# Optimization experiments

Measured on AMD Instinct MI355X. Metric: run time of the kernel, lower is better.

The kernel has to match this reference:

```python
import jax, jax.numpy as jnp
import numpy as np


def _pool2(x):
    # 2x2 max pool, stride 2 (matches F.max_pool2d(x, 2))
    b, c, h, w = x.shape
    return x.reshape(b, c, h // 2, 2, w // 2, 2).max(axis=(3, 5))


def setup_inputs() -> dict:
    key = jax.random.key(0)
    ks = jax.random.split(key, 6)
    B, C, H, W = 16, 512, 64, 64
    x = jax.random.normal(ks[0], (B, C, H, W), dtype=jnp.float32)
    scale = 0.02
    theta_w = jax.random.normal(ks[1], (C // 8, C), dtype=jnp.float32) * scale
    phi_w = jax.random.normal(ks[2], (C // 8, C), dtype=jnp.float32) * scale
    g_w = jax.random.normal(ks[3], (C // 2, C), dtype=jnp.float32) * scale
    o_w = jax.random.normal(ks[4], (C, C // 2), dtype=jnp.float32) * scale
    # original inits gamma=0; use a nonzero value so output depends on attention path
    gamma = jax.random.normal(ks[5], (), dtype=jnp.float32) * 0.5
    return {"x": x, "theta_w": theta_w, "phi_w": phi_w, "g_w": g_w, "o_w": o_w, "gamma": gamma}


def reference(x, theta_w, phi_w, g_w, o_w, gamma):
    B, C, H, W = x.shape
    HW = H * W
    # 1x1 convs == channel GEMMs
    theta = jnp.einsum('bchw,kc->bkhw', x, theta_w).reshape(B, C // 8, HW).transpose(0, 2, 1)  # [B, HW, C/8]
    phi = _pool2(jnp.einsum('bchw,kc->bkhw', x, phi_w)).reshape(B, C // 8, HW // 4)            # [B, C/8, HW/4]
    beta = jax.nn.softmax(jnp.einsum('bnk,bkm->bnm', theta, phi), axis=-1)                     # [B, HW, HW/4]
    g = _pool2(jnp.einsum('bchw,kc->bkhw', x, g_w)).reshape(B, C // 2, HW // 4)                # [B, C/2, HW/4]
    # g.bmm(beta^T): contract over pooled positions m -> [B, C/2, HW]
    o_in = jnp.einsum('bcm,bnm->bcn', g, beta).reshape(B, C // 2, H, W)
    o = jnp.einsum('bchw,kc->bkhw', o_in, o_w)                                                 # [B, C, H, W]
    return gamma * o + x
```

## Files before the change

kernel.cpp:

```cpp
#include <hip/hip_runtime.h>

#define B_   16
#define C_   512
#define HW_  4096
#define M_   1024
#define TPAD 136

typedef __attribute__((ext_vector_type(8))) short bf16x8;
typedef __attribute__((ext_vector_type(4))) float f32x4;

static __device__ __forceinline__ unsigned short f2bf(float f) {
    union { float f; unsigned u; } v; v.f = f;
    unsigned r = v.u + 0x7fffu + ((v.u >> 16) & 1u);
    return (unsigned short)(r >> 16);
}
static __device__ __forceinline__ float bf2f(unsigned short h) {
    union { unsigned u; float f; } v; v.u = ((unsigned)h) << 16;
    return v.f;
}
static __device__ __forceinline__ void gload_lds16(const void* g, void* l) {
    __builtin_amdgcn_global_load_lds(
        (const __attribute__((address_space(1))) unsigned int*)g,
        (__attribute__((address_space(3))) unsigned int*)l, 16, 0, 0);
}

__global__ __launch_bounds__(256) void k_weights(
    const float* __restrict__ thw, const float* __restrict__ phw,
    const float* __restrict__ gw,  const float* __restrict__ ow,
    unsigned short* __restrict__ Wb, unsigned short* __restrict__ oWb) {
    int i = blockIdx.x * 256 + threadIdx.x;
    if (i < 32768)        Wb[i] = f2bf(thw[i]);
    else if (i < 65536)   Wb[i] = f2bf(phw[i - 32768]);
    else if (i < 196608)  Wb[i] = f2bf(gw[i - 65536]);
    else if (i < 327680)  oWb[i - 196608] = f2bf(ow[i - 196608]);
}

__global__ __launch_bounds__(256) void k_transpose_x(
    const float* __restrict__ x, unsigned short* __restrict__ xT) {
    __shared__ float tile[64][65];
    int b = blockIdx.z, c0 = blockIdx.y * 64, hw0 = blockIdx.x * 64;
    const float* xb = x + ((size_t)b * C_ + c0) * HW_ + hw0;
    int t = threadIdx.x;
    int r = t >> 4, c4 = (t & 15) * 4;
#pragma unroll
    for (int k = 0; k < 4; k++) {
        int row = r + k * 16;
        float4 v = *reinterpret_cast<const float4*>(xb + (size_t)row * HW_ + c4);
        tile[row][c4 + 0] = v.x; tile[row][c4 + 1] = v.y;
        tile[row][c4 + 2] = v.z; tile[row][c4 + 3] = v.w;
    }
    __syncthreads();
    unsigned short* o = xT + ((size_t)b * HW_ + hw0) * C_ + c0;
#pragma unroll
    for (int k = 0; k < 4; k++) {
        int hwr = r + k * 16;
        ushort4 u;
        u.x = f2bf(tile[c4 + 0][hwr]); u.y = f2bf(tile[c4 + 1][hwr]);
        u.z = f2bf(tile[c4 + 2][hwr]); u.w = f2bf(tile[c4 + 3][hwr]);
        *reinterpret_cast<ushort4*>(o + (size_t)hwr * C_ + c4) = u;
    }
}

__global__ __launch_bounds__(256, 4) void k_proj(
    const unsigned short* __restrict__ xT, const unsigned short* __restrict__ Wb,
    unsigned short* __restrict__ theta_n, unsigned short* __restrict__ phi_p,
    unsigned short* __restrict__ g_p) {
    __shared__ unsigned short smem[128 * TPAD];
    unsigned short* As = smem;
    unsigned short* Bs = smem + 8192;

    int b = blockIdx.z, mt = blockIdx.y, bx = blockIdx.x;
    int hw0 = bx * 128;
    int tid = threadIdx.x, w = tid >> 6, lane = tid & 63;
    int l15 = lane & 15, q = lane >> 4;
    int wr = w >> 1, wc = w & 1;

    const unsigned short* Ab = Wb + (size_t)(mt * 128) * 512;
    const unsigned short* Bb = xT + ((size_t)b * HW_ + hw0) * 512;
    int trow = tid >> 3, tch = tid & 7;

    f32x4 acc[4][4] = {};
    for (int ks = 0; ks < 8; ks++) {
        int k0 = ks * 64;
        if (ks) __syncthreads();
#pragma unroll
        for (int i = 0; i < 4; i++) {
            int row = i * 32 + trow;
            int ch = tch ^ (row & 7);
            gload_lds16(Ab + (size_t)row * 512 + k0 + ch * 8, &As[(i * 256 + w * 64) * 8]);
        }
#pragma unroll
        for (int i = 0; i < 4; i++) {
            int row = i * 32 + trow;
            int ch = tch ^ (row & 7);
            gload_lds16(Bb + (size_t)row * 512 + k0 + ch * 8, &Bs[(i * 256 + w * 64) * 8]);
        }
        __syncthreads();
#pragma unroll
        for (int kk = 0; kk < 2; kk++) {
            bf16x8 af[4], bfr[4];
#pragma unroll
            for (int mi = 0; mi < 4; mi++) {
                int row = wr * 64 + mi * 16 + l15;
                int ch = (kk * 4 + q) ^ (row & 7);
                af[mi] = *(const bf16x8*)&As[row * 64 + ch * 8];
            }
#pragma unroll
            for (int ni = 0; ni < 4; ni++) {
                int row = wc * 64 + ni * 16 + l15;
                int ch = (kk * 4 + q) ^ (row & 7);
                bfr[ni] = *(const bf16x8*)&Bs[row * 64 + ch * 8];
            }
#pragma unroll
            for (int mi = 0; mi < 4; mi++)
#pragma unroll
                for (int ni = 0; ni < 4; ni++)
                    acc[mi][ni] = __builtin_amdgcn_mfma_f32_16x16x32_bf16(
                        af[mi], bfr[ni], acc[mi][ni], 0, 0, 0);
        }
    }

    __syncthreads();
#pragma unroll
    for (int mi = 0; mi < 4; mi++)
#pragma unroll
        for (int ni = 0; ni < 4; ni++) {
            int col = wc * 64 + ni * 16 + l15;
            int row = wr * 64 + mi * 16 + q * 4;
            ushort4 u;
            u.x = f2bf(acc[mi][ni][0]); u.y = f2bf(acc[mi][ni][1]);
            u.z = f2bf(acc[mi][ni][2]); u.w = f2bf(acc[mi][ni][3]);
            *reinterpret_cast<ushort4*>(&smem[col * TPAD + row]) = u;
        }
    __syncthreads();

    if (mt == 0) {
        int hw_l = tid >> 1, kh = (tid & 1) * 32;
        const unsigned short* srcp = &smem[hw_l * TPAD + kh];
        unsigned short* dstp = theta_n + ((size_t)b * HW_ + hw0 + hw_l) * 64 + kh;
#pragma unroll
        for (int i = 0; i < 4; i++)
            *reinterpret_cast<uint4*>(dstp + i * 8) =
                *reinterpret_cast<const uint4*>(srcp + i * 8);
        int pc = tid & 63, mg = tid >> 6;
#pragma unroll
        for (int j = 0; j < 8; j++) {
            int m_l = mg * 8 + j, w_ = m_l * 2;
            float v0 = bf2f(smem[(w_)      * TPAD + 64 + pc]);
            float v1 = bf2f(smem[(w_ + 1)  * TPAD + 64 + pc]);
            float v2 = bf2f(smem[(64 + w_) * TPAD + 64 + pc]);
            float v3 = bf2f(smem[(65 + w_) * TPAD + 64 + pc]);
            float v = fmaxf(fmaxf(v0, v1), fmaxf(v2, v3));
            phi_p[((size_t)b * M_ + bx * 32 + m_l) * 64 + pc] = f2bf(v);
        }
    } else {
        int lr = tid & 127, half = tid >> 7;
        int gc = (mt - 1) * 128 + lr;
        unsigned short* dst = g_p + ((size_t)b * 256 + gc) * M_ + bx * 32 + half * 16;
        unsigned short tmp[16];
#pragma unroll
        for (int i = 0; i < 16; i++) {
            int w_ = (half * 16 + i) * 2;
            float v0 = bf2f(smem[(w_)      * TPAD + lr]);
            float v1 = bf2f(smem[(w_ + 1)  * TPAD + lr]);
            float v2 = bf2f(smem[(64 + w_) * TPAD + lr]);
            float v3 = bf2f(smem[(65 + w_) * TPAD + lr]);
            tmp[i] = f2bf(fmaxf(fmaxf(v0, v1), fmaxf(v2, v3)));
        }
#pragma unroll
        for (int i = 0; i < 4; i++)
            *reinterpret_cast<ushort4*>(dst + i * 4) =
                *reinterpret_cast<const ushort4*>(&tmp[i * 4]);
    }
}

__global__ __launch_bounds__(256, 2) void k_attn(
    const unsigned short* __restrict__ theta_n, const unsigned short* __restrict__ phi_p,
    const unsigned short* __restrict__ g_p, unsigned short* __restrict__ o_in) {
    __shared__ unsigned short phi_s[64 * 64];
    __shared__ unsigned short g_s[256 * 64];
    __shared__ unsigned short p_lds[4][32][68];

    int b = blockIdx.y, n0 = blockIdx.x * 128;
    int tid = threadIdx.x, w = tid >> 6, lane = tid & 63;
    int l15 = lane & 15, q = lane >> 4;
    int nw = n0 + w * 32;

    const unsigned short* th = theta_n + ((size_t)b * HW_ + nw + l15) * 64 + q * 8;
    bf16x8 a[2][2];
    a[0][0] = *(const bf16x8*)(th);            a[0][1] = *(const bf16x8*)(th + 32);
    a[1][0] = *(const bf16x8*)(th + 16 * 64);  a[1][1] = *(const bf16x8*)(th + 16 * 64 + 32);

    const unsigned short* phib = phi_p + (size_t)b * M_ * 64;
    const unsigned short* gb   = g_p   + (size_t)b * 256 * M_;

    bf16x8 ones;
    {
        short v = (l15 == 0) ? (short)0x3F80 : (short)0;
#pragma unroll
        for (int i = 0; i < 8; i++) ones[i] = v;
    }

    int sw = l15 & 7;

    f32x4 acc[2][17] = {};
    for (int mc = 0; mc < 16; mc++) {
        int m0 = mc * 64;
        __syncthreads();
#pragma unroll
        for (int i = 0; i < 2; i++) {
            int u = i * 256 + tid;
            int row = u >> 3, ch = (lane & 7) ^ (row & 7);
            gload_lds16(phib + (size_t)(m0 + row) * 64 + ch * 8,
                        &phi_s[(i * 256 + w * 64) * 8]);
        }
#pragma unroll
        for (int i = 0; i < 8; i++) {
            int u = i * 256 + tid;
            int row = u >> 3, ch = (lane & 7) ^ (row & 7);
            gload_lds16(gb + (size_t)row * M_ + m0 + ch * 8,
                        &g_s[(i * 256 + w * 64) * 8]);
        }
        __syncthreads();

#pragma unroll
        for (int f = 0; f < 4; f++) {
            const unsigned short* pr = &phi_s[(f * 16 + l15) * 64];
            bf16x8 b0 = *(const bf16x8*)(pr + (q ^ sw) * 8);
            bf16x8 b1 = *(const bf16x8*)(pr + ((q + 4) ^ sw) * 8);
#pragma unroll
            for (int t = 0; t < 2; t++) {
                f32x4 s = {};
                s = __builtin_amdgcn_mfma_f32_16x16x32_bf16(a[t][0], b0, s, 0, 0, 0);
                s = __builtin_amdgcn_mfma_f32_16x16x32_bf16(a[t][1], b1, s, 0, 0, 0);
#pragma unroll
                for (int j = 0; j < 4; j++)
                    p_lds[w][t * 16 + q * 4 + j][f * 16 + l15] = f2bf(__expf(s[j]));
            }
        }
        bf16x8 p[2][2];
#pragma unroll
        for (int t = 0; t < 2; t++) {
            p[t][0] = *(const bf16x8*)&p_lds[w][t * 16 + l15][q * 8];
            p[t][1] = *(const bf16x8*)&p_lds[w][t * 16 + l15][32 + q * 8];
        }
#pragma unroll
        for (int cf = 0; cf < 16; cf++) {
            const unsigned short* gr = &g_s[(cf * 16 + l15) * 64];
            bf16x8 g0 = *(const bf16x8*)(gr + (q ^ sw) * 8);
            bf16x8 g1 = *(const bf16x8*)(gr + ((q + 4) ^ sw) * 8);
#pragma unroll
            for (int t = 0; t < 2; t++) {
                acc[t][cf] = __builtin_amdgcn_mfma_f32_16x16x32_bf16(p[t][0], g0, acc[t][cf], 0, 0, 0);
                acc[t][cf] = __builtin_amdgcn_mfma_f32_16x16x32_bf16(p[t][1], g1, acc[t][cf], 0, 0, 0);
            }
        }
#pragma unroll
        for (int t = 0; t < 2; t++) {
            acc[t][16] = __builtin_amdgcn_mfma_f32_16x16x32_bf16(p[t][0], ones, acc[t][16], 0, 0, 0);
            acc[t][16] = __builtin_amdgcn_mfma_f32_16x16x32_bf16(p[t][1], ones, acc[t][16], 0, 0, 0);
        }
    }

#pragma unroll
    for (int t = 0; t < 2; t++) {
        float dinv[4];
#pragma unroll
        for (int j = 0; j < 4; j++) {
            float d = __shfl(acc[t][16][j], (lane & 48), 64);
            dinv[j] = 1.0f / d;
        }
#pragma unroll
        for (int cf = 0; cf < 16; cf++)
#pragma unroll
            for (int j = 0; j < 4; j++)
                o_in[((size_t)b * HW_ + nw + t * 16 + q * 4 + j) * 256 + cf * 16 + l15] =
                    f2bf(acc[t][cf][j] * dinv[j]);
    }
}

__global__ __launch_bounds__(256, 4) void k_oproj(
    const unsigned short* __restrict__ o_in, const unsigned short* __restrict__ oWb,
    const float* __restrict__ x, const float* __restrict__ gamma_p,
    float* __restrict__ out) {
    __shared__ unsigned short smem[128 * TPAD];
    unsigned short* As = smem;
    unsigned short* Bs = smem + 8192;

    int b = blockIdx.z, mt = blockIdx.y, hw0 = blockIdx.x * 128;
    int tid = threadIdx.x, w = tid >> 6, lane = tid & 63;
    int l15 = lane & 15, q = lane >> 4;
    int wr = w >> 1, wc = w & 1;

    const unsigned short* Ab = oWb + (size_t)(mt * 128) * 256;
    const unsigned short* Bb = o_in + ((size_t)b * HW_ + hw0) * 256;
    int trow = tid >> 3, tch = tid & 7;

    f32x4 acc[4][4] = {};
    for (int ks = 0; ks < 4; ks++) {
        int k0 = ks * 64;
        if (ks) __syncthreads();
#pragma unroll
        for (int i = 0; i < 4; i++) {
            int row = i * 32 + trow;
            int ch = tch ^ (row & 7);
            gload_lds16(Ab + (size_t)row * 256 + k0 + ch * 8, &As[(i * 256 + w * 64) * 8]);
        }
#pragma unroll
        for (int i = 0; i < 4; i++) {
            int row = i * 32 + trow;
            int ch = tch ^ (row & 7);
            gload_lds16(Bb + (size_t)row * 256 + k0 + ch * 8, &Bs[(i * 256 + w * 64) * 8]);
        }
        __syncthreads();
#pragma unroll
        for (int kk = 0; kk < 2; kk++) {
            bf16x8 af[4], bfr[4];
#pragma unroll
            for (int mi = 0; mi < 4; mi++) {
                int row = wr * 64 + mi * 16 + l15;
                int ch = (kk * 4 + q) ^ (row & 7);
                af[mi] = *(const bf16x8*)&As[row * 64 + ch * 8];
            }
#pragma unroll
            for (int ni = 0; ni < 4; ni++) {
                int row = wc * 64 + ni * 16 + l15;
                int ch = (kk * 4 + q) ^ (row & 7);
                bfr[ni] = *(const bf16x8*)&Bs[row * 64 + ch * 8];
            }
#pragma unroll
            for (int mi = 0; mi < 4; mi++)
#pragma unroll
                for (int ni = 0; ni < 4; ni++)
                    acc[mi][ni] = __builtin_amdgcn_mfma_f32_16x16x32_bf16(
                        af[mi], bfr[ni], acc[mi][ni], 0, 0, 0);
        }
    }

    __syncthreads();
#pragma unroll
    for (int mi = 0; mi < 4; mi++)
#pragma unroll
        for (int ni = 0; ni < 4; ni++) {
            int col = wc * 64 + ni * 16 + l15;
            int rb = wr * 64 + mi * 16 + q * 4;
#pragma unroll
            for (int j = 0; j < 4; j++)
                smem[(rb + j) * TPAD + col] = f2bf(acc[mi][ni][j]);
        }
    __syncthreads();

    float gam = *gamma_p;
    int sub = tid >> 5, p32 = tid & 31;
#pragma unroll
    for (int p = 0; p < 16; p++) {
        int row = p * 8 + sub;
        ushort4 v = *reinterpret_cast<const ushort4*>(&smem[row * TPAD + p32 * 4]);
        size_t idx = ((size_t)b * C_ + mt * 128 + row) * HW_ + hw0 + p32 * 4;
        float4 xv = *reinterpret_cast<const float4*>(x + idx);
        float4 o;
        o.x = gam * bf2f(v.x) + xv.x;
        o.y = gam * bf2f(v.y) + xv.y;
        o.z = gam * bf2f(v.z) + xv.z;
        o.w = gam * bf2f(v.w) + xv.w;
        *reinterpret_cast<float4*>(out + idx) = o;
    }
}

extern "C" void kernel_launch(void* const* d_in, const int* in_sizes, int n_in,
                              void* d_out, int out_size, void* d_ws, size_t ws_size,
                              hipStream_t stream) {
    const float* x     = (const float*)d_in[0];
    const float* thw   = (const float*)d_in[1];
    const float* phw   = (const float*)d_in[2];
    const float* gw    = (const float*)d_in[3];
    const float* ow    = (const float*)d_in[4];
    const float* gamma = (const float*)d_in[5];
    float* out = (float*)d_out;

    char* ws = (char*)d_ws;
    unsigned short* xT   = (unsigned short*)(ws + 0);
    unsigned short* Wb   = (unsigned short*)(ws + 67108864);
    unsigned short* oWb  = (unsigned short*)(ws + 67502080);
    unsigned short* oin  = (unsigned short*)(ws + 67764224);
    unsigned short* thn  = (unsigned short*)(ws + 101318656);
    unsigned short* phip = (unsigned short*)(ws + 109707264);
    unsigned short* gp   = (unsigned short*)(ws + 111804416);

    hipLaunchKernelGGL(k_weights, dim3(1280), dim3(256), 0, stream, thw, phw, gw, ow, Wb, oWb);
    hipLaunchKernelGGL(k_transpose_x, dim3(64, 8, 16), dim3(256), 0, stream, x, xT);
    hipLaunchKernelGGL(k_proj, dim3(32, 3, 16), dim3(256), 0, stream, xT, Wb, thn, phip, gp);
    hipLaunchKernelGGL(k_attn, dim3(32, 16), dim3(256), 0, stream, thn, phip, gp, oin);
    hipLaunchKernelGGL(k_oproj, dim3(32, 4, 16), dim3(256), 0, stream, oin, oWb, x, gamma, out);
}
```

Before: 192.3 us.

## Fuse x transpose and bf16 cast into projection GEMM with double-buffered fp32 staging

Removes the separate transpose kernel and its bf16 xT buffer. The projection kernel now stages fp32 x tiles directly into double-buffered LDS and converts them to bf16 in registers with v_cvt_pk_bf16_f32. One 512-thread block now computes all 384 output rows (theta, phi, g) for an hw tile, so each x tile is read once instead of three times. Weights are read straight from global memory into registers, and the epilogue writes the three output slices in sequence. In exchange, LDS use per block is higher and register pressure rises with 6x4 accumulators.

```diff
diff --git a/kernel.cpp b/kernel.cpp
--- a/kernel.cpp
+++ b/kernel.cpp
@@ -22,6 +22,11 @@
     __builtin_amdgcn_global_load_lds(
         (const __attribute__((address_space(1))) unsigned int*)g,
         (__attribute__((address_space(3))) unsigned int*)l, 16, 0, 0);
+}
+static __device__ __forceinline__ unsigned cvt_pk(float lo, float hi) {
+    unsigned r;
+    asm("v_cvt_pk_bf16_f32 %0, %1, %2" : "=v"(r) : "v"(lo), "v"(hi));
+    return r;
 }
 
 __global__ __launch_bounds__(256) void k_weights(
@@ -35,142 +40,121 @@
     else if (i < 327680)  oWb[i - 196608] = f2bf(ow[i - 196608]);
 }
 
-__global__ __launch_bounds__(256) void k_transpose_x(
-    const float* __restrict__ x, unsigned short* __restrict__ xT) {
-    __shared__ float tile[64][65];
-    int b = blockIdx.z, c0 = blockIdx.y * 64, hw0 = blockIdx.x * 64;
-    const float* xb = x + ((size_t)b * C_ + c0) * HW_ + hw0;
-    int t = threadIdx.x;
-    int r = t >> 4, c4 = (t & 15) * 4;
-#pragma unroll
-    for (int k = 0; k < 4; k++) {
-        int row = r + k * 16;
-        float4 v = *reinterpret_cast<const float4*>(xb + (size_t)row * HW_ + c4);
-        tile[row][c4 + 0] = v.x; tile[row][c4 + 1] = v.y;
-        tile[row][c4 + 2] = v.z; tile[row][c4 + 3] = v.w;
-    }
-    __syncthreads();
-    unsigned short* o = xT + ((size_t)b * HW_ + hw0) * C_ + c0;
-#pragma unroll
-    for (int k = 0; k < 4; k++) {
-        int hwr = r + k * 16;
-        ushort4 u;
-        u.x = f2bf(tile[c4 + 0][hwr]); u.y = f2bf(tile[c4 + 1][hwr]);
-        u.z = f2bf(tile[c4 + 2][hwr]); u.w = f2bf(tile[c4 + 3][hwr]);
-        *reinterpret_cast<ushort4*>(o + (size_t)hwr * C_ + c4) = u;
-    }
-}
-
-__global__ __launch_bounds__(256, 4) void k_proj(
-    const unsigned short* __restrict__ xT, const unsigned short* __restrict__ Wb,
+__global__ __launch_bounds__(512, 2) void k_proj(
+    const float* __restrict__ x, const unsigned short* __restrict__ Wb,
     unsigned short* __restrict__ theta_n, unsigned short* __restrict__ phi_p,
     unsigned short* __restrict__ g_p) {
+    __shared__ float xlds[2][64 * 128];
     __shared__ unsigned short smem[128 * TPAD];
-    unsigned short* As = smem;
-    unsigned short* Bs = smem + 8192;
-
-    int b = blockIdx.z, mt = blockIdx.y, bx = blockIdx.x;
+
+    int b = blockIdx.y, bx = blockIdx.x;
     int hw0 = bx * 128;
     int tid = threadIdx.x, w = tid >> 6, lane = tid & 63;
     int l15 = lane & 15, q = lane >> 4;
-    int wr = w >> 1, wc = w & 1;
-
-    const unsigned short* Ab = Wb + (size_t)(mt * 128) * 512;
-    const unsigned short* Bb = xT + ((size_t)b * HW_ + hw0) * 512;
-    int trow = tid >> 3, tch = tid & 7;
-
-    f32x4 acc[4][4] = {};
+    int rg = w >> 1, cg = w & 1;
+
+    const float* xb = x + (size_t)b * C_ * HW_ + hw0;
+
+#define STAGEX(ks_, buf_)                                                      \
+    _Pragma("unroll")                                                          \
+    for (int i = 0; i < 4; i++) {                                              \
+        int u = i * 512 + tid;                                                 \
+        int c = u >> 5, chunk = u & 31;                                        \
+        int swz = ((c >> 3) & 1) << 4;                                         \
+        gload_lds16(xb + (size_t)((ks_) * 64 + c) * HW_ + ((chunk * 4) ^ swz), \
+                    &xlds[buf_][(i * 512 + w * 64) * 4]);                      \
+    }
+
+    STAGEX(0, 0);
+    __syncthreads();
+
+    f32x4 acc[6][4] = {};
     for (int ks = 0; ks < 8; ks++) {
-        int k0 = ks * 64;
-        if (ks) __syncthreads();
-#pragma unroll
-        for (int i = 0; i < 4; i++) {
-            int row = i * 32 + trow;
-            int ch = tch ^ (row & 7);
-            gload_lds16(Ab + (size_t)row * 512 + k0 + ch * 8, &As[(i * 256 + w * 64) * 8]);
-        }
-#pragma unroll
-        for (int i = 0; i < 4; i++) {
-            int row = i * 32 + trow;
-            int ch = tch ^ (row & 7);
-            gload_lds16(Bb + (size_t)row * 512 + k0 + ch * 8, &Bs[(i * 256 + w * 64) * 8]);
-        }
-        __syncthreads();
+        int cur = ks & 1;
+        bf16x8 af[2][6];
+#pragma unroll
+        for (int kk = 0; kk < 2; kk++)
+#pragma unroll
+            for (int mi = 0; mi < 6; mi++) {
+                int row = rg * 96 + mi * 16 + l15;
+                af[kk][mi] = *(const bf16x8*)(Wb + (size_t)row * 512 + ks * 64 + kk * 32 + q * 8);
+            }
+        if (ks < 7) { STAGEX(ks + 1, cur ^ 1); }
 #pragma unroll
         for (int kk = 0; kk < 2; kk++) {
-            bf16x8 af[4], bfr[4];
-#pragma unroll
-            for (int mi = 0; mi < 4; mi++) {
-                int row = wr * 64 + mi * 16 + l15;
-                int ch = (kk * 4 + q) ^ (row & 7);
-                af[mi] = *(const bf16x8*)&As[row * 64 + ch * 8];
-            }
 #pragma unroll
             for (int ni = 0; ni < 4; ni++) {
-                int row = wc * 64 + ni * 16 + l15;
-                int ch = (kk * 4 + q) ^ (row & 7);
-                bfr[ni] = *(const bf16x8*)&Bs[row * 64 + ch * 8];
-            }
-#pragma unroll
-            for (int mi = 0; mi < 4; mi++)
-#pragma unroll
-                for (int ni = 0; ni < 4; ni++)
+                int colsw = (cg * 64 + ni * 16 + l15) ^ ((q & 1) << 4);
+                const float* base = &xlds[cur][(kk * 32 + q * 8) * 128 + colsw];
+                float f0 = base[0],   f1 = base[128], f2 = base[256], f3 = base[384];
+                float f4 = base[512], f5 = base[640], f6 = base[768], f7 = base[896];
+                bf16x8 bfr;
+                unsigned* bw = (unsigned*)&bfr;
+                bw[0] = cvt_pk(f0, f1); bw[1] = cvt_pk(f2, f3);
+                bw[2] = cvt_pk(f4, f5); bw[3] = cvt_pk(f6, f7);
+#pragma unroll
+                for (int mi = 0; mi < 6; mi++)
                     acc[mi][ni] = __builtin_amdgcn_mfma_f32_16x16x32_bf16(
-                        af[mi], bfr[ni], acc[mi][ni], 0, 0, 0);
-        }
-    }
-
-    __syncthreads();
-#pragma unroll
-    for (int mi = 0; mi < 4; mi++)
-#pragma unroll
-        for (int ni = 0; ni < 4; ni++) {
-            int col = wc * 64 + ni * 16 + l15;
-            int row = wr * 64 + mi * 16 + q * 4;
-            ushort4 u;
-            u.x = f2bf(acc[mi][ni][0]); u.y = f2bf(acc[mi][ni][1]);
-            u.z = f2bf(acc[mi][ni][2]); u.w = f2bf(acc[mi][ni][3]);
-            *reinterpret_cast<ushort4*>(&smem[col * TPAD + row]) = u;
-        }
-    __syncthreads();
-
-    if (mt == 0) {
-        int hw_l = tid >> 1, kh = (tid & 1) * 32;
-        const unsigned short* srcp = &smem[hw_l * TPAD + kh];
-        unsigned short* dstp = theta_n + ((size_t)b * HW_ + hw0 + hw_l) * 64 + kh;
-#pragma unroll
-        for (int i = 0; i < 4; i++)
-            *reinterpret_cast<uint4*>(dstp + i * 8) =
-                *reinterpret_cast<const uint4*>(srcp + i * 8);
-        int pc = tid & 63, mg = tid >> 6;
-#pragma unroll
-        for (int j = 0; j < 8; j++) {
-            int m_l = mg * 8 + j, w_ = m_l * 2;
-            float v0 = bf2f(smem[(w_)      * TPAD + 64 + pc]);
-            float v1 = bf2f(smem[(w_ + 1)  * TPAD + 64 + pc]);
-            float v2 = bf2f(smem[(64 + w_) * TPAD + 64 + pc]);
-            float v3 = bf2f(smem[(65 + w_) * TPAD + 64 + pc]);
-            float v = fmaxf(fmaxf(v0, v1), fmaxf(v2, v3));
-            phi_p[((size_t)b * M_ + bx * 32 + m_l) * 64 + pc] = f2bf(v);
-        }
-    } else {
-        int lr = tid & 127, half = tid >> 7;
-        int gc = (mt - 1) * 128 + lr;
-        unsigned short* dst = g_p + ((size_t)b * 256 + gc) * M_ + bx * 32 + half * 16;
-        unsigned short tmp[16];
-#pragma unroll
-        for (int i = 0; i < 16; i++) {
-            int w_ = (half * 16 + i) * 2;
-            float v0 = bf2f(smem[(w_)      * TPAD + lr]);
-            float v1 = bf2f(smem[(w_ + 1)  * TPAD + lr]);
-            float v2 = bf2f(smem[(64 + w_) * TPAD + lr]);
-            float v3 = bf2f(smem[(65 + w_) * TPAD + lr]);
-            tmp[i] = f2bf(fmaxf(fmaxf(v0, v1), fmaxf(v2, v3)));
-        }
-#pragma unroll
-        for (int i = 0; i < 4; i++)
-            *reinterpret_cast<ushort4*>(dst + i * 4) =
-                *reinterpret_cast<const ushort4*>(&tmp[i * 4]);
+                        af[kk][mi], bfr, acc[mi][ni], 0, 0, 0);
+            }
+        }
+        __syncthreads();
+    }
+#undef STAGEX
+
+    for (int t = 0; t < 3; t++) {
+        __syncthreads();
+#pragma unroll
+        for (int mi = 0; mi < 6; mi++) {
+            int grow = rg * 96 + mi * 16;
+            if ((grow >> 7) == t) {
+#pragma unroll
+                for (int ni = 0; ni < 4; ni++) {
+                    int col = cg * 64 + ni * 16 + l15;
+                    int row = (grow & 127) + q * 4;
+                    ushort4 u;
+                    u.x = f2bf(acc[mi][ni][0]); u.y = f2bf(acc[mi][ni][1]);
+                    u.z = f2bf(acc[mi][ni][2]); u.w = f2bf(acc[mi][ni][3]);
+                    *reinterpret_cast<ushort4*>(&smem[col * TPAD + row]) = u;
+                }
+            }
+        }
+        __syncthreads();
+
+        if (t == 0) {
+            int hw_l = tid >> 2, kh = (tid & 3) * 16;
+            const unsigned short* srcp = &smem[hw_l * TPAD + kh];
+            unsigned short* dstp = theta_n + ((size_t)b * HW_ + hw0 + hw_l) * 64 + kh;
+            *reinterpret_cast<uint4*>(dstp)     = *reinterpret_cast<const uint4*>(srcp);
+            *reinterpret_cast<uint4*>(dstp + 8) = *reinterpret_cast<const uint4*>(srcp + 8);
+            int pc = tid & 63, mg = tid >> 6;
+#pragma unroll
+            for (int j = 0; j < 4; j++) {
+                int m_l = mg * 4 + j, w_ = m_l * 2;
+                float v0 = bf2f(smem[(w_)      * TPAD + 64 + pc]);
+                float v1 = bf2f(smem[(w_ + 1)  * TPAD + 64 + pc]);
+                float v2 = bf2f(smem[(64 + w_) * TPAD + 64 + pc]);
+                float v3 = bf2f(smem[(65 + w_) * TPAD + 64 + pc]);
+                float v = fmaxf(fmaxf(v0, v1), fmaxf(v2, v3));
+                phi_p[((size_t)b * M_ + bx * 32 + m_l) * 64 + pc] = f2bf(v);
+            }
+        } else {
+            int lr = tid & 127, mq = tid >> 7;
+            int gc = (t - 1) * 128 + lr;
+            unsigned short* dst = g_p + ((size_t)b * 256 + gc) * M_ + bx * 32 + mq * 8;
+            unsigned short tmp[8];
+#pragma unroll
+            for (int i = 0; i < 8; i++) {
+                int w_ = (mq * 8 + i) * 2;
+                float v0 = bf2f(smem[(w_)      * TPAD + lr]);
+                float v1 = bf2f(smem[(w_ + 1)  * TPAD + lr]);
+                float v2 = bf2f(smem[(64 + w_) * TPAD + lr]);
+                float v3 = bf2f(smem[(65 + w_) * TPAD + lr]);
+                tmp[i] = f2bf(fmaxf(fmaxf(v0, v1), fmaxf(v2, v3)));
+            }
+            *reinterpret_cast<ushort4*>(dst)     = *reinterpret_cast<const ushort4*>(&tmp[0]);
+            *reinterpret_cast<ushort4*>(dst + 4) = *reinterpret_cast<const ushort4*>(&tmp[4]);
+        }
     }
 }
 
@@ -379,17 +363,15 @@
     float* out = (float*)d_out;
 
     char* ws = (char*)d_ws;
-    unsigned short* xT   = (unsigned short*)(ws + 0);
-    unsigned short* Wb   = (unsigned short*)(ws + 67108864);
-    unsigned short* oWb  = (unsigned short*)(ws + 67502080);
-    unsigned short* oin  = (unsigned short*)(ws + 67764224);
-    unsigned short* thn  = (unsigned short*)(ws + 101318656);
-    unsigned short* phip = (unsigned short*)(ws + 109707264);
-    unsigned short* gp   = (unsigned short*)(ws + 111804416);
+    unsigned short* Wb   = (unsigned short*)(ws + 0);
+    unsigned short* oWb  = (unsigned short*)(ws + 393216);
+    unsigned short* oin  = (unsigned short*)(ws + 655360);
+    unsigned short* thn  = (unsigned short*)(ws + 34209792);
+    unsigned short* phip = (unsigned short*)(ws + 42598400);
+    unsigned short* gp   = (unsigned short*)(ws + 44695552);
 
     hipLaunchKernelGGL(k_weights, dim3(1280), dim3(256), 0, stream, thw, phw, gw, ow, Wb, oWb);
-    hipLaunchKernelGGL(k_transpose_x, dim3(64, 8, 16), dim3(256), 0, stream, x, xT);
-    hipLaunchKernelGGL(k_proj, dim3(32, 3, 16), dim3(256), 0, stream, xT, Wb, thn, phip, gp);
+    hipLaunchKernelGGL(k_proj, dim3(32, 16), dim3(512), 0, stream, x, Wb, thn, phip, gp);
     hipLaunchKernelGGL(k_attn, dim3(32, 16), dim3(256), 0, stream, thn, phip, gp, oin);
     hipLaunchKernelGGL(k_oproj, dim3(32, 4, 16), dim3(256), 0, stream, oin, oWb, x, gamma, out);
 }
```

After: 192.2 us. About the same (-0.1%).
